# Kernel tuning notes

Hardware: AMD Instinct MI355X
Metric: run time of the kernel (lower is better)

Reference implementation:

```python
import jax, jax.numpy as jnp
import numpy as np

NUM_HEADS = 16

def setup_inputs() -> dict:
    key = jax.random.key(0)
    ks = jax.random.split(key, 9)
    E = 1024
    T, B = 2048, 2
    s = E ** -0.5
    return {
        "query": jax.random.normal(ks[0], (T, B, E), dtype=jnp.float32),
        "Wq": jax.random.normal(ks[1], (E, E), dtype=jnp.float32) * s,
        "bq": jax.random.normal(ks[2], (E,), dtype=jnp.float32) * 0.02,
        "Wk": jax.random.normal(ks[3], (E, E), dtype=jnp.float32) * s,
        "bk": jax.random.normal(ks[4], (E,), dtype=jnp.float32) * 0.02,
        "Wv": jax.random.normal(ks[5], (E, E), dtype=jnp.float32) * s,
        "bv": jax.random.normal(ks[6], (E,), dtype=jnp.float32) * 0.02,
        "Wo": jax.random.normal(ks[7], (E, E), dtype=jnp.float32) * s,
        "bo": jax.random.normal(ks[8], (E,), dtype=jnp.float32) * 0.02,
    }

def reference(query, Wq, bq, Wk, bk, Wv, bv, Wo, bo):
    # query: [T, B, E] (seq-first, fairseq/ESM layout)
    T, B, E = query.shape
    H = NUM_HEADS
    D = E // H
    scaling = D ** -0.5
    # projections (eqx Linear: x @ W.T + b); note k/v also come from `query` (self-attention)
    q = (query @ Wq.T + bq) * scaling
    k = query @ Wk.T + bk
    v = query @ Wv.T + bv
    # [T, B, E] -> [B*H, T, D]
    q = q.reshape(T, B * H, D).transpose(1, 0, 2)
    k = k.reshape(T, B * H, D).transpose(1, 0, 2)
    v = v.reshape(T, B * H, D).transpose(1, 0, 2)
    # full score matrix [B*H, T, T], softmax in fp32 (as in original)
    scores = jnp.einsum('ntd,nsd->nts', q, k)
    attn_w = jax.nn.softmax(scores.astype(jnp.float32), axis=-1)
    attn = jnp.einsum('nts,nsd->ntd', attn_w.astype(v.dtype), v)
    # [B*H, T, D] -> [T, B, E]
    attn = attn.transpose(1, 0, 2).reshape(T, B, E)
    return attn @ Wo.T + bo
```

## Files before the change

### kernel.cpp

```cpp
#include <hip/hip_runtime.h>
#include <hip/hip_bf16.h>


typedef __attribute__((ext_vector_type(8))) short short8;
typedef __attribute__((ext_vector_type(4))) float f32x4;
typedef __attribute__((ext_vector_type(16))) float f32x16;
typedef __attribute__((ext_vector_type(4))) unsigned u32x4;

#define T_DIM 2048
#define B_DIM 2
#define E_DIM 1024
#define H_DIM 16
#define D_DIM 64
#define M_ROWS (T_DIM * B_DIM)
#define QKV_N (3 * E_DIM)
#define HEAD_ELEMS (32 * 2048 * 64)
#define LOG2E 1.44269504088896340736f

__device__ __forceinline__ unsigned short f2bf(float f) {
    unsigned u = __builtin_bit_cast(unsigned, f);
    unsigned r = (u + 0x7fffu + ((u >> 16) & 1u)) >> 16;
    return (unsigned short)r;
}

__device__ __forceinline__ unsigned cvt_pk_bf16(float lo, float hi) {
    unsigned d;
    asm("v_cvt_pk_bf16_f32 %0, %1, %2" : "=v"(d) : "v"(lo), "v"(hi));
    return d;
}

__device__ __forceinline__ void gload_lds16(const void* g, void* l) {
    __builtin_amdgcn_global_load_lds(
        (const __attribute__((address_space(1))) void*)g,
        (__attribute__((address_space(3))) void*)l, 16, 0, 0);
}

__device__ __forceinline__ f32x16 mfma32(short8 a, short8 b, f32x16 c) {
    return __builtin_amdgcn_mfma_f32_32x32x16_bf16(a, b, c, 0, 0, 0);
}

__global__ __launch_bounds__(256) void cast_all(
    const float* __restrict__ X,
    const float* __restrict__ Wq, const float* __restrict__ Wk,
    const float* __restrict__ Wv, const float* __restrict__ Wo,
    unsigned short* __restrict__ Xbf,
    unsigned short* __restrict__ Wcat,
    unsigned short* __restrict__ Wobf)
{
    int idx = blockIdx.x * 256 + threadIdx.x;
    size_t base = (size_t)idx * 8;
    int row = (int)(base >> 10);
    int col = (int)(base & 1023);
    const float* src;
    unsigned short* dst;
    float scale = 1.0f;
    if (row < 4096) {
        src = X + base;
        dst = Xbf + base;
    } else if (row < 7168) {
        int wrow = row - 4096;
        if (wrow < 1024)      { src = Wq + ((size_t)wrow << 10) + col; scale = 0.125f * LOG2E; }
        else if (wrow < 2048) { src = Wk + ((size_t)(wrow - 1024) << 10) + col; }
        else                  { src = Wv + ((size_t)(wrow - 2048) << 10) + col; }
        dst = Wcat + ((size_t)wrow << 10) + col;
    } else {
        int wrow = row - 7168;
        src = Wo + ((size_t)wrow << 10) + col;
        dst = Wobf + ((size_t)wrow << 10) + col;
    }
    float4 f0 = *(const float4*)src;
    float4 f1 = *(const float4*)(src + 4);
    short8 r;
    r[0] = (short)f2bf(f0.x * scale);
    r[1] = (short)f2bf(f0.y * scale);
    r[2] = (short)f2bf(f0.z * scale);
    r[3] = (short)f2bf(f0.w * scale);
    r[4] = (short)f2bf(f1.x * scale);
    r[5] = (short)f2bf(f1.y * scale);
    r[6] = (short)f2bf(f1.z * scale);
    r[7] = (short)f2bf(f1.w * scale);
    *(short8*)dst = r;
}

__global__ __launch_bounds__(256) void bias_fuse(
    const float* __restrict__ bq, const float* __restrict__ bk,
    const float* __restrict__ bv, float* __restrict__ biasq)
{
    int i = blockIdx.x * 256 + threadIdx.x;
    if (i < 1024)       biasq[i] = 0.125f * LOG2E * bq[i];
    else if (i < 2048)  biasq[i] = bk[i - 1024];
    else if (i < 3072)  biasq[i] = bv[i - 2048];
}

template <int MODE>
__global__ __launch_bounds__(256) void gemm_bt(
    const unsigned short* __restrict__ A,
    const unsigned short* __restrict__ B,
    const float* __restrict__ bias,
    void* __restrict__ outp,
    int M, int N, int K)
{
    __shared__ alignas(16) unsigned short As[128 * 32];
    __shared__ alignas(16) unsigned short Bs[128 * 32];
    const int tid = threadIdx.x;
    const int wave = tid >> 6, lane = tid & 63;
    const int lr = lane & 15, lg = lane >> 4;
    const int nbx = N >> 7;
    const int bx = blockIdx.x % nbx, by = blockIdx.x / nbx;
    const int wr = wave >> 1, wc = wave & 1;

    f32x4 acc[4][4] = {};

    for (int kt = 0; kt < K; kt += 32) {
        for (int pass = 0; pass < 2; ++pass) {
            int c = pass * 256 + wave * 64 + lane;
            int row = c >> 2, kc = c & 3;
            const unsigned short* srcA = A + (size_t)(by * 128 + row) * K + kt + kc * 8;
            const unsigned short* srcB = B + (size_t)(bx * 128 + row) * K + kt + kc * 8;
            char* dstA = (char*)As + (pass * 256 + wave * 64) * 16;
            char* dstB = (char*)Bs + (pass * 256 + wave * 64) * 16;
            gload_lds16(srcA, dstA);
            gload_lds16(srcB, dstB);
        }
        __syncthreads();
        short8 af[4], bf[4];
#pragma unroll
        for (int m = 0; m < 4; ++m)
            af[m] = *(const short8*)&As[(wr * 64 + m * 16 + lr) * 32 + lg * 8];
#pragma unroll
        for (int n = 0; n < 4; ++n)
            bf[n] = *(const short8*)&Bs[(wc * 64 + n * 16 + lr) * 32 + lg * 8];
#pragma unroll
        for (int m = 0; m < 4; ++m)
#pragma unroll
            for (int n = 0; n < 4; ++n)
                acc[m][n] = __builtin_amdgcn_mfma_f32_16x16x32_bf16(af[m], bf[n], acc[m][n], 0, 0, 0);
        __syncthreads();
    }

    const int gcol0 = bx * 128 + wc * 64;
    const int grow0 = by * 128 + wr * 64;
    if (MODE == 0) {
        unsigned short* qb = (unsigned short*)outp;
#pragma unroll
        for (int m = 0; m < 4; ++m) {
#pragma unroll
            for (int n = 0; n < 4; ++n) {
                int col = gcol0 + n * 16 + lr;
                float bsv = bias[col];
                int which = col >> 10;
                int e = col & 1023;
                int h = e >> 6, d = e & 63;
                if (which < 2) {
                    unsigned short* bufb = qb + (size_t)which * HEAD_ELEMS;
#pragma unroll
                    for (int j = 0; j < 4; ++j) {
                        int r = grow0 + m * 16 + lg * 4 + j;
                        int t = r >> 1, b = r & 1;
                        int bh = b * 16 + h;
                        bufb[((size_t)bh * 2048 + t) * 64 + d] = f2bf(acc[m][n][j] + bsv);
                    }
                } else {
                    unsigned* vT32 = (unsigned*)(qb + (size_t)2 * HEAD_ELEMS);
                    int t0 = (grow0 + m * 16 + lg * 4) >> 1;
                    int dwidx = t0 >> 1;
                    int dwp = (dwidx & ~6) | ((dwidx & 2) << 1) | ((dwidx & 4) >> 1);
                    unsigned w0 = (unsigned)f2bf(acc[m][n][0] + bsv) |
                                  ((unsigned)f2bf(acc[m][n][2] + bsv) << 16);
                    unsigned w1 = (unsigned)f2bf(acc[m][n][1] + bsv) |
                                  ((unsigned)f2bf(acc[m][n][3] + bsv) << 16);
                    vT32[(size_t)(h * 64 + d) * 1024 + dwp] = w0;
                    vT32[(size_t)((16 + h) * 64 + d) * 1024 + dwp] = w1;
                }
            }
        }
    } else {
        float* O = (float*)outp;
#pragma unroll
        for (int m = 0; m < 4; ++m) {
#pragma unroll
            for (int n = 0; n < 4; ++n) {
                int col = gcol0 + n * 16 + lr;
                float bsv = bias[col];
#pragma unroll
                for (int j = 0; j < 4; ++j) {
                    int r = grow0 + m * 16 + lg * 4 + j;
                    O[(size_t)r * N + col] = acc[m][n][j] + bsv;
                }
            }
        }
    }
}

struct AttnCtx {
    const unsigned short* kh;
    const unsigned short* vh;
    int tid, ql, hi;
};

template<bool DO_PV>
__device__ __forceinline__ void attn_step(
    const AttnCtx& cx, int t,
    unsigned short (*Ks)[64 * 64], unsigned short (*Vs)[64 * 64],
    const short8 (&qv)[4],
    const short8 (&vfP)[8], const short8 (&paP)[4],
    short8 (&vfC)[8], short8 (&paC)[4],
    f32x16 (&accO)[2], float& lrun)
{
    const int buf = t & 1;
    const int tid = cx.tid, ql = cx.ql, hi = cx.hi;
    if (t < 31) {
        const int kt = (t + 1) * 64;
#pragma unroll
        for (int p = 0; p < 2; ++p) {
            int c = p * 256 + tid;
            int row = c >> 3;
            int sxb = ((c & 7) * 16) ^ ((row & 7) << 4);
            gload_lds16(cx.kh + (size_t)(kt + row) * 64 + (sxb >> 1),
                        (char*)&Ks[buf ^ 1][0] + c * 16);
        }
#pragma unroll
        for (int p = 0; p < 2; ++p) {
            int c = p * 256 + tid;
            int d = c >> 3;
            int sxb = ((c & 7) * 16) ^ ((d & 7) << 4);
            gload_lds16(cx.vh + (size_t)d * 2048 + kt + (sxb >> 1),
                        (char*)&Vs[buf ^ 1][0] + c * 16);
        }
        asm volatile("s_waitcnt vmcnt(4)" ::: "memory");
    } else {
        asm volatile("s_waitcnt vmcnt(0)" ::: "memory");
    }
    __builtin_amdgcn_s_barrier();
    __builtin_amdgcn_sched_barrier(0);

    const char* Kb = (const char*)&Ks[buf][0];
    const char* Vb = (const char*)&Vs[buf][0];

    f32x16 st[2] = {};
    __builtin_amdgcn_s_setprio(1);
#pragma unroll
    for (int m = 0; m < 2; ++m) {
        int krow = m * 32 + ql;
#pragma unroll
        for (int c = 0; c < 4; ++c) {
            int bo = (krow * 128 + c * 32 + hi * 16) ^ ((krow & 7) << 4);
            short8 ka = *(const short8*)(Kb + bo);
            st[m] = mfma32(ka, qv[c], st[m]);
        }
    }
#pragma unroll
    for (int n = 0; n < 2; ++n) {
        int d = n * 32 + ql;
#pragma unroll
        for (int kc = 0; kc < 4; ++kc) {
            int bo = (d * 128 + kc * 32 + hi * 16) ^ ((d & 7) << 4);
            vfC[n * 4 + kc] = *(const short8*)(Vb + bo);
        }
    }
    if constexpr (DO_PV) {
#pragma unroll
        for (int n = 0; n < 2; ++n)
#pragma unroll
            for (int kc = 0; kc < 4; ++kc)
                accO[n] = mfma32(vfP[n * 4 + kc], paP[kc], accO[n]);
    }
    __builtin_amdgcn_s_setprio(0);
    __builtin_amdgcn_sched_barrier(0);

    float rs = 0.0f;
#pragma unroll
    for (int m = 0; m < 2; ++m)
#pragma unroll
        for (int r = 0; r < 16; ++r) {
            float e = __builtin_amdgcn_exp2f(st[m][r]);
            st[m][r] = e;
            rs += e;
        }
    lrun += rs;

#pragma unroll
    for (int kc = 0; kc < 4; ++kc) {
        int m = kc >> 1, b8 = (kc & 1) * 8;
        u32x4 u;
        u[0] = cvt_pk_bf16(st[m][b8 + 0], st[m][b8 + 1]);
        u[1] = cvt_pk_bf16(st[m][b8 + 2], st[m][b8 + 3]);
        u[2] = cvt_pk_bf16(st[m][b8 + 4], st[m][b8 + 5]);
        u[3] = cvt_pk_bf16(st[m][b8 + 6], st[m][b8 + 7]);
        paC[kc] = __builtin_bit_cast(short8, u);
    }

    asm volatile("s_waitcnt lgkmcnt(0)" ::: "memory");
    __builtin_amdgcn_sched_barrier(0);
    __builtin_amdgcn_s_barrier();
}

__global__ __launch_bounds__(256, 2) void attn_fwd(
    const unsigned short* __restrict__ q,
    const unsigned short* __restrict__ k,
    const unsigned short* __restrict__ vT,
    unsigned short* __restrict__ outb)
{
    __shared__ alignas(16) unsigned short Ks[2][64 * 64];
    __shared__ alignas(16) unsigned short Vs[2][64 * 64];
    const int tid = threadIdx.x, wv = tid >> 6, l = tid & 63;
    const int ql = l & 31, hi = l >> 5;
    const int lid = blockIdx.x;
    const int xcd = lid & 7, slot = lid >> 3;
    const int bh = xcd * 4 + (slot >> 4);
    const int q0 = (slot & 15) * 128;
    const unsigned short* qh = q + (size_t)bh * (2048 * 64);
    AttnCtx cx;
    cx.kh = k + (size_t)bh * (2048 * 64);
    cx.vh = vT + (size_t)bh * (64 * 2048);
    cx.tid = tid; cx.ql = ql; cx.hi = hi;

    const int qrow = q0 + wv * 32 + ql;
    short8 qv[4];
#pragma unroll
    for (int c = 0; c < 4; ++c)
        qv[c] = *(const short8*)&qh[(size_t)qrow * 64 + c * 16 + hi * 8];

    f32x16 accO[2] = {};
    float lrun = 0.0f;
    short8 vfA[8], vfB[8], paA[4], paB[4];

    {
#pragma unroll
        for (int p = 0; p < 2; ++p) {
            int c = p * 256 + tid;
            int row = c >> 3;
            int sxb = ((c & 7) * 16) ^ ((row & 7) << 4);
            gload_lds16(cx.kh + (size_t)row * 64 + (sxb >> 1),
                        (char*)&Ks[0][0] + c * 16);
        }
#pragma unroll
        for (int p = 0; p < 2; ++p) {
            int c = p * 256 + tid;
            int d = c >> 3;
            int sxb = ((c & 7) * 16) ^ ((d & 7) << 4);
            gload_lds16(cx.vh + (size_t)d * 2048 + (sxb >> 1),
                        (char*)&Vs[0][0] + c * 16);
        }
    }

    attn_step<false>(cx, 0, Ks, Vs, qv, vfB, paB, vfA, paA, accO, lrun);
    for (int t = 1; t < 31; t += 2) {
        attn_step<true>(cx, t,     Ks, Vs, qv, vfA, paA, vfB, paB, accO, lrun);
        attn_step<true>(cx, t + 1, Ks, Vs, qv, vfB, paB, vfA, paA, accO, lrun);
    }
    attn_step<true>(cx, 31, Ks, Vs, qv, vfA, paA, vfB, paB, accO, lrun);
#pragma unroll
    for (int n = 0; n < 2; ++n)
#pragma unroll
        for (int kc = 0; kc < 4; ++kc)
            accO[n] = mfma32(vfB[n * 4 + kc], paB[kc], accO[n]);

    const float ltot = lrun + __shfl_xor(lrun, 32);
    const float inv = 1.0f / ltot;
    const int b = bh >> 4, h = bh & 15;
    const int orow = qrow * 2 + b;
#pragma unroll
    for (int n = 0; n < 2; ++n)
#pragma unroll
        for (int rq = 0; rq < 4; ++rq) {
            uint2 u;
            u.x = cvt_pk_bf16(accO[n][rq * 4 + 0] * inv, accO[n][rq * 4 + 1] * inv);
            u.y = cvt_pk_bf16(accO[n][rq * 4 + 2] * inv, accO[n][rq * 4 + 3] * inv);
            *(uint2*)&outb[(size_t)orow * 1024 + h * 64 + n * 32 + rq * 8 + hi * 4] = u;
        }
}

extern "C" void kernel_launch(void* const* d_in, const int* in_sizes, int n_in,
                              void* d_out, int out_size, void* d_ws, size_t ws_size,
                              hipStream_t stream) {
    const float* X  = (const float*)d_in[0];
    const float* Wq = (const float*)d_in[1];
    const float* bq = (const float*)d_in[2];
    const float* Wk = (const float*)d_in[3];
    const float* bk = (const float*)d_in[4];
    const float* Wv = (const float*)d_in[5];
    const float* bv = (const float*)d_in[6];
    const float* Wo = (const float*)d_in[7];
    const float* bo = (const float*)d_in[8];
    float* out = (float*)d_out;

    char* ws = (char*)d_ws;
    if (ws_size < ((size_t)49 << 20)) return;
    unsigned short* Xbf   = (unsigned short*)(ws);
    unsigned short* Wcat  = (unsigned short*)(ws + ((size_t)8  << 20));
    unsigned short* Wobf  = (unsigned short*)(ws + ((size_t)14 << 20));
    unsigned short* qb    = (unsigned short*)(ws + ((size_t)16 << 20));
    unsigned short* ab    = (unsigned short*)(ws + ((size_t)40 << 20));
    float*          biasq = (float*)(ws + ((size_t)48 << 20));
    unsigned short* kb  = qb + (size_t)HEAD_ELEMS;
    unsigned short* vTb = qb + (size_t)2 * HEAD_ELEMS;

    cast_all<<<4096, 256, 0, stream>>>(X, Wq, Wk, Wv, Wo, Xbf, Wcat, Wobf);
    bias_fuse<<<12, 256, 0, stream>>>(bq, bk, bv, biasq);
    gemm_bt<0><<<dim3((M_ROWS / 128) * (QKV_N / 128)), 256, 0, stream>>>(
        Xbf, Wcat, biasq, (void*)qb, M_ROWS, QKV_N, E_DIM);
    attn_fwd<<<dim3(32 * 16), 256, 0, stream>>>(qb, kb, vTb, ab);
    gemm_bt<1><<<dim3((M_ROWS / 128) * (E_DIM / 128)), 256, 0, stream>>>(
        ab, Wobf, bo, (void*)out, M_ROWS, E_DIM, E_DIM);
}
```

Measured before the change: 123.9 us.

## Double-buffer LDS tiles in projection GEMM to overlap global loads with MFMA

```diff
diff --git a/kernel.cpp b/kernel.cpp
--- a/kernel.cpp
+++ b/kernel.cpp
@@ -100,8 +100,8 @@
     void* __restrict__ outp,
     int M, int N, int K)
 {
-    __shared__ alignas(16) unsigned short As[128 * 32];
-    __shared__ alignas(16) unsigned short Bs[128 * 32];
+    __shared__ alignas(16) unsigned short As[2][128 * 32];
+    __shared__ alignas(16) unsigned short Bs[2][128 * 32];
     const int tid = threadIdx.x;
     const int wave = tid >> 6, lane = tid & 63;
     const int lr = lane & 15, lg = lane >> 4;
@@ -111,31 +111,49 @@
 
     f32x4 acc[4][4] = {};
 
-    for (int kt = 0; kt < K; kt += 32) {
+    auto stage = [&](int buf, int kt) {
+#pragma unroll
         for (int pass = 0; pass < 2; ++pass) {
             int c = pass * 256 + wave * 64 + lane;
             int row = c >> 2, kc = c & 3;
-            const unsigned short* srcA = A + (size_t)(by * 128 + row) * K + kt + kc * 8;
-            const unsigned short* srcB = B + (size_t)(bx * 128 + row) * K + kt + kc * 8;
-            char* dstA = (char*)As + (pass * 256 + wave * 64) * 16;
-            char* dstB = (char*)Bs + (pass * 256 + wave * 64) * 16;
-            gload_lds16(srcA, dstA);
-            gload_lds16(srcB, dstB);
-        }
-        __syncthreads();
+            gload_lds16(A + (size_t)(by * 128 + row) * K + kt + kc * 8,
+                        (char*)&As[buf][0] + c * 16);
+            gload_lds16(B + (size_t)(bx * 128 + row) * K + kt + kc * 8,
+                        (char*)&Bs[buf][0] + c * 16);
+        }
+    };
+
+    const int NK = K >> 5;
+    stage(0, 0);
+    for (int ki = 0; ki < NK; ++ki) {
+        const int buf = ki & 1;
+        if (ki < NK - 1) {
+            stage(buf ^ 1, (ki + 1) * 32);
+            asm volatile("s_waitcnt vmcnt(4)" ::: "memory");
+        } else {
+            asm volatile("s_waitcnt vmcnt(0)" ::: "memory");
+        }
+        __builtin_amdgcn_s_barrier();
+        __builtin_amdgcn_sched_barrier(0);
+
         short8 af[4], bf[4];
 #pragma unroll
         for (int m = 0; m < 4; ++m)
-            af[m] = *(const short8*)&As[(wr * 64 + m * 16 + lr) * 32 + lg * 8];
+            af[m] = *(const short8*)&As[buf][(wr * 64 + m * 16 + lr) * 32 + lg * 8];
 #pragma unroll
         for (int n = 0; n < 4; ++n)
-            bf[n] = *(const short8*)&Bs[(wc * 64 + n * 16 + lr) * 32 + lg * 8];
+            bf[n] = *(const short8*)&Bs[buf][(wc * 64 + n * 16 + lr) * 32 + lg * 8];
+        __builtin_amdgcn_s_setprio(1);
 #pragma unroll
         for (int m = 0; m < 4; ++m)
 #pragma unroll
             for (int n = 0; n < 4; ++n)
                 acc[m][n] = __builtin_amdgcn_mfma_f32_16x16x32_bf16(af[m], bf[n], acc[m][n], 0, 0, 0);
-        __syncthreads();
+        __builtin_amdgcn_s_setprio(0);
+
+        asm volatile("s_waitcnt lgkmcnt(0)" ::: "memory");
+        __builtin_amdgcn_sched_barrier(0);
+        __builtin_amdgcn_s_barrier();
     }
 
     const int gcol0 = bx * 128 + wc * 64;
```

After: 117.4 us. 5.3% less time.
